# Optimization experiments

Measured on AMD Instinct MI355X. Metric: run time of the kernel, lower is better.

The kernel has to match this reference:

```python
import jax, jax.numpy as jnp
import numpy as np

B, T, I, H, L = 64, 1024, 64, 512, 2


def setup_inputs() -> dict:
    key = jax.random.key(0)
    ks = jax.random.split(key, 4 * L + 4)
    k = 1.0 / np.sqrt(H)
    inp = {"x": jax.random.normal(ks[0], (B, T, I), dtype=jnp.float32)}
    in_sizes = [I] + [H] * (L - 1)
    for l in range(L):
        base = 1 + 4 * l
        inp[f"w_ih{l}"] = jax.random.uniform(ks[base + 0], (3 * H, in_sizes[l]), minval=-k, maxval=k, dtype=jnp.float32)
        inp[f"w_hh{l}"] = jax.random.uniform(ks[base + 1], (3 * H, H), minval=-k, maxval=k, dtype=jnp.float32)
        inp[f"b_ih{l}"] = jax.random.uniform(ks[base + 2], (3 * H,), minval=-k, maxval=k, dtype=jnp.float32)
        inp[f"b_hh{l}"] = jax.random.uniform(ks[base + 3], (3 * H,), minval=-k, maxval=k, dtype=jnp.float32)
    kf = 1.0 / np.sqrt(H)
    inp["fc_w"] = jax.random.uniform(ks[-2], (I, H), minval=-kf, maxval=kf, dtype=jnp.float32)
    inp["fc_b"] = jax.random.uniform(ks[-1], (I,), minval=-kf, maxval=kf, dtype=jnp.float32)
    return inp


def _gru_layer(x, w_ih, w_hh, b_ih, b_hh):
    # x: [B, T, in]; precompute input-side gates as one big GEMM
    xg = jnp.einsum('bti,gi->btg', x, w_ih) + b_ih  # [B, T, 3H]
    h0 = jnp.zeros((x.shape[0], w_hh.shape[1]), x.dtype)

    def step(h, xg_t):
        hg = h @ w_hh.T + b_hh                     # [B, 3H]
        xr, xz, xn = jnp.split(xg_t, 3, axis=-1)
        hr, hz, hn = jnp.split(hg, 3, axis=-1)
        r = jax.nn.sigmoid(xr + hr)
        z = jax.nn.sigmoid(xz + hz)
        n = jnp.tanh(xn + r * hn)
        h_new = (1.0 - z) * n + z * h
        return h_new, h_new

    _, ys = jax.lax.scan(step, h0, jnp.swapaxes(xg, 0, 1))  # ys: [T, B, H]
    return jnp.swapaxes(ys, 0, 1)


def reference(x, w_ih0, w_hh0, b_ih0, b_hh0, w_ih1, w_hh1, b_ih1, b_hh1, fc_w, fc_b):
    h = _gru_layer(x, w_ih0, w_hh0, b_ih0, b_hh0)
    h = _gru_layer(h, w_ih1, w_hh1, b_ih1, b_hh1)
    return h @ fc_w.T + fc_b
```

## Files before the change

### kernel.cpp

```cpp
#include <hip/hip_runtime.h>
#include <hip/hip_bf16.h>

#define T_TOTAL 1024
#define BATCH   64
#define HID     512

__device__ __forceinline__ float fast_sigmoid(float x) {
    return 1.f / (1.f + __expf(-x));
}
__device__ __forceinline__ float fast_tanh(float x) {
    float ax = fabsf(x);
    float e  = __expf(-2.f * ax);
    float t  = (1.f - e) / (1.f + e);
    return copysignf(t, x);
}

template<int BM, int BN, int TM, int TN>
__global__ __launch_bounds__(256, 2)
void gemm_bt_k(const float* __restrict__ A, const float* __restrict__ W,
               const float* __restrict__ bias, float* __restrict__ C,
               int K, int T, int Tc, int t0, int N)
{
    constexpr int BK = 16;
    constexpr int WSTR = BN + (BN / 32) * 4;
    static_assert(BM / TM == 16 && BN / TN == 16, "256 threads required");
    __shared__ float As[BK][BM + 4];
    __shared__ float Ws[BK][WSTR];

    const int tid = threadIdx.x;
    const int tx  = tid & 15;
    const int ty  = tid >> 4;
    const int m0  = blockIdx.y * BM;
    const int n0  = blockIdx.x * BN;
    const int nA  = tx * TN;
    const int nsw = nA + ((nA >> 5) << 2);

    float acc[TM][TN];
#pragma unroll
    for (int i = 0; i < TM; ++i)
#pragma unroll
        for (int j = 0; j < TN; ++j) acc[i][j] = 0.f;

    for (int k0 = 0; k0 < K; k0 += BK) {
#pragma unroll
        for (int i = 0; i < (BM * BK) / 1024; ++i) {
            int id = tid + (i << 8);
            int m  = id >> 2;
            int kq = (id & 3) << 2;
            int mloc = m0 + m;
            int rowg = (mloc / Tc) * T + t0 + (mloc % Tc);
            const float4 v = *reinterpret_cast<const float4*>(A + (size_t)rowg * K + k0 + kq);
            As[kq + 0][m] = v.x; As[kq + 1][m] = v.y;
            As[kq + 2][m] = v.z; As[kq + 3][m] = v.w;
        }
#pragma unroll
        for (int i = 0; i < (BN * BK) / 1024; ++i) {
            int id = tid + (i << 8);
            int n  = id >> 2;
            int kq = (id & 3) << 2;
            const float4 v = *reinterpret_cast<const float4*>(W + (size_t)(n0 + n) * K + k0 + kq);
            int np = n + ((n >> 5) << 2);
            Ws[kq + 0][np] = v.x; Ws[kq + 1][np] = v.y;
            Ws[kq + 2][np] = v.z; Ws[kq + 3][np] = v.w;
        }
        __syncthreads();
#pragma unroll
        for (int k = 0; k < BK; ++k) {
            float a[TM], b[TN];
#pragma unroll
            for (int i = 0; i < TM; i += 4)
                *reinterpret_cast<float4*>(&a[i]) =
                    *reinterpret_cast<const float4*>(&As[k][ty * TM + i]);
#pragma unroll
            for (int j = 0; j < TN; j += 4)
                *reinterpret_cast<float4*>(&b[j]) =
                    *reinterpret_cast<const float4*>(&Ws[k][nsw + j]);
#pragma unroll
            for (int i = 0; i < TM; ++i)
#pragma unroll
                for (int j = 0; j < TN; ++j)
                    acc[i][j] = fmaf(a[i], b[j], acc[i][j]);
        }
        __syncthreads();
    }
#pragma unroll
    for (int i = 0; i < TM; ++i) {
        const size_t crow = (size_t)(m0 + ty * TM + i) * N + n0 + nA;
#pragma unroll
        for (int j = 0; j < TN; j += 4) {
            float4 bv = *reinterpret_cast<const float4*>(bias + n0 + nA + j);
            float4 v;
            v.x = acc[i][j + 0] + bv.x; v.y = acc[i][j + 1] + bv.y;
            v.z = acc[i][j + 2] + bv.z; v.w = acc[i][j + 3] + bv.w;
            *reinterpret_cast<float4*>(C + crow + j) = v;
        }
    }
}

__global__ __launch_bounds__(512, 2)
void gru_scan(const float* __restrict__ xg,
              const float* __restrict__ w_hh,
              const float* __restrict__ b_hh,
              float* __restrict__ y,
              unsigned long long* __restrict__ hbuf,
              int t0, int Tc, int tagbase)
{
    const int tid = threadIdx.x;
    const int grp = blockIdx.x & 31;
    const int os  = blockIdx.x >> 5;
    const int D0  = os << 6;
    const int d   = tid & 63;
    const int kc  = tid >> 6;
    const int bg  = grp << 1;

    constexpr int HP = 528;
    __shared__ float h_lds[2][2 * HP];
    __shared__ float part[8 * 392];
    __shared__ float hg_red[392];

    float4 w4[3][16];
#pragma unroll
    for (int g = 0; g < 3; ++g) {
        const float* wr = w_hh + (size_t)(g * 512 + D0 + d) * 512 + kc * 64;
#pragma unroll
        for (int j = 0; j < 16; ++j)
            w4[g][j] = *reinterpret_cast<const float4*>(wr + (j << 2));
    }
    float bias0 = (tid < 384) ? b_hh[(tid >> 7) * 512 + D0 + (tid & 63)] : 0.f;
    const int b_loc = tid >> 6;

    for (int tl = 0; tl < Tc; ++tl) {
        const int tg = t0 + tl;
        float* hl = h_lds[tl & 1];

        float xr = 0.f, xz = 0.f, xn = 0.f;
        if (tid < 128) {
            const size_t rowo = ((size_t)(bg + b_loc) * Tc + tl) * 1536 + D0 + d;
            xr = xg[rowo];
            xz = xg[rowo + 512];
            xn = xg[rowo + 1024];
        }

        if (tg == 0) {
#pragma unroll
            for (int i = 0; i < 2; ++i) {
                int idx = tid + (i << 9);
                hl[(idx >> 9) * HP + (idx & 511)] = 0.f;
            }
        } else {
            const unsigned long long* hsrc =
                hbuf + (size_t)(grp * 2 + ((tg - 1) & 1)) * 1024;
            const unsigned int tagexp = (unsigned int)(tagbase + tl - 1);
            unsigned long long v[2];
            unsigned int pend = 0x3u;
            while (pend) {
#pragma unroll
                for (int i = 0; i < 2; ++i)
                    if (pend & (1u << i))
                        v[i] = __hip_atomic_load(hsrc + tid + (i << 9),
                                __ATOMIC_RELAXED, __HIP_MEMORY_SCOPE_AGENT);
#pragma unroll
                for (int i = 0; i < 2; ++i)
                    if ((pend & (1u << i)) &&
                        (unsigned int)(v[i] >> 32) == tagexp) {
                        int idx = tid + (i << 9);
                        union { unsigned int u; float f; } cv;
                        cv.u = (unsigned int)v[i];
                        hl[(idx >> 9) * HP + (idx & 511)] = cv.f;
                        pend &= ~(1u << i);
                    }
                if (pend) __builtin_amdgcn_s_sleep(1);
            }
        }
        __syncthreads();

        float acc[3][2];
#pragma unroll
        for (int g = 0; g < 3; ++g) { acc[g][0] = 0.f; acc[g][1] = 0.f; }
        const float* hb_base = hl + kc * 64;
#pragma unroll
        for (int j = 0; j < 16; ++j) {
            const float4 h0 = *reinterpret_cast<const float4*>(hb_base + (j << 2));
            const float4 h1 = *reinterpret_cast<const float4*>(hb_base + HP + (j << 2));
#pragma unroll
            for (int g = 0; g < 3; ++g) {
                const float4 wv = w4[g][j];
                acc[g][0] = fmaf(wv.x, h0.x, acc[g][0]);
                acc[g][0] = fmaf(wv.y, h0.y, acc[g][0]);
                acc[g][0] = fmaf(wv.z, h0.z, acc[g][0]);
                acc[g][0] = fmaf(wv.w, h0.w, acc[g][0]);
                acc[g][1] = fmaf(wv.x, h1.x, acc[g][1]);
                acc[g][1] = fmaf(wv.y, h1.y, acc[g][1]);
                acc[g][1] = fmaf(wv.z, h1.z, acc[g][1]);
                acc[g][1] = fmaf(wv.w, h1.w, acc[g][1]);
            }
        }
        {
            float* pp = part + kc * 392 + d;
#pragma unroll
            for (int g = 0; g < 3; ++g) {
                pp[g * 128]      = acc[g][0];
                pp[g * 128 + 64] = acc[g][1];
            }
        }
        __syncthreads();

        if (tid < 384) {
            float s = bias0;
#pragma unroll
            for (int q = 0; q < 8; ++q) s += part[q * 392 + tid];
            hg_red[tid] = s;
        }
        __syncthreads();

        if (tid < 128) {
            const float hr = hg_red[tid];
            const float hz = hg_red[128 + tid];
            const float hn = hg_red[256 + tid];
            const int D = D0 + d;
            const float hp = hl[b_loc * HP + D];
            const float r = fast_sigmoid(xr + hr);
            const float z = fast_sigmoid(xz + hz);
            const float nv = fast_tanh(xn + r * hn);
            const float h = (1.f - z) * nv + z * hp;
            union { float f; unsigned int u; } cv; cv.f = h;
            const unsigned long long pk =
                ((unsigned long long)(unsigned int)(tagbase + tl) << 32) | cv.u;
            unsigned long long* hdst =
                hbuf + (size_t)(grp * 2 + (tg & 1)) * 1024 + b_loc * 512 + D;
            __hip_atomic_store(hdst, pk, __ATOMIC_RELAXED,
                               __HIP_MEMORY_SCOPE_AGENT);
            y[((size_t)(bg + b_loc) * T_TOTAL + tg) * HID + D] = h;
        }
    }
}

extern "C" void kernel_launch(void* const* d_in, const int* in_sizes, int n_in,
                              void* d_out, int out_size, void* d_ws, size_t ws_size,
                              hipStream_t stream)
{
    const float* x       = (const float*)d_in[0];
    const float* w_ih[2] = {(const float*)d_in[1], (const float*)d_in[5]};
    const float* w_hh[2] = {(const float*)d_in[2], (const float*)d_in[6]};
    const float* b_ih[2] = {(const float*)d_in[3], (const float*)d_in[7]};
    const float* b_hh[2] = {(const float*)d_in[4], (const float*)d_in[8]};
    const float* fc_w    = (const float*)d_in[9];
    const float* fc_b    = (const float*)d_in[10];
    float* out = (float*)d_out;

    const size_t Y_BYTES = (size_t)BATCH * T_TOTAL * HID * 4;
    const size_t H_BYTES = (size_t)32 * 2 * 2 * 512 * 8;
    int Tc = 256;
    while (Tc > 32) {
        size_t need = (size_t)BATCH * Tc * 1536 * 4 + Y_BYTES + H_BYTES;
        if (need <= ws_size) break;
        Tc >>= 1;
    }

    char* p = (char*)d_ws;
    float* xg_buf = (float*)p;                 p += (size_t)BATCH * Tc * 1536 * 4;
    float* y_buf  = (float*)p;                 p += Y_BYTES;
    unsigned long long* hbuf = (unsigned long long*)p;

    const int nchunks = T_TOTAL / Tc;
    for (int L = 0; L < 2; ++L) {
        const float* A = L ? y_buf : x;
        const int K    = L ? HID : 64;
        for (int c = 0; c < nchunks; ++c) {
            dim3 g1(1536 / 128, (BATCH * Tc) / 128);
            gemm_bt_k<128, 128, 8, 8><<<g1, 256, 0, stream>>>(
                A, w_ih[L], b_ih[L], xg_buf, K, T_TOTAL, Tc, c * Tc, 1536);
            gru_scan<<<256, 512, 0, stream>>>(
                xg_buf, w_hh[L], b_hh[L], y_buf, hbuf,
                c * Tc, Tc, (L << 11) + c * Tc);
        }
    }
    dim3 g2(64 / 64, (BATCH * T_TOTAL) / 128);
    gemm_bt_k<128, 64, 8, 4><<<g2, 256, 0, stream>>>(
        y_buf, fc_w, fc_b, out, HID, BATCH * T_TOTAL, BATCH * T_TOTAL, 0, 64);
}
```

Measured before the change: 6.952 ms.

## Add per-group arrival counter for scan sync and fold gate reduction into epilogue

Adds a per-group atomic arrival counter. Each gate-computing wavefront increments it after its stores have drained. One thread per block spins on the counter with s_sleep before the rest of the block reads the tagged hidden state, which is meant to cut heavy polling traffic on hbuf. The separate 384-thread partial-sum reduction and its __syncthreads are also removed: the 128 gate threads now sum all three gates' partials themselves. The trade-off is an extra block barrier and sleep latency on the critical path of every timestep, plus more serial work on the gate threads.

```diff
diff --git a/kernel.cpp b/kernel.cpp
--- a/kernel.cpp
+++ b/kernel.cpp
@@ -103,7 +103,8 @@
               const float* __restrict__ b_hh,
               float* __restrict__ y,
               unsigned long long* __restrict__ hbuf,
-              int t0, int Tc, int tagbase)
+              unsigned int* __restrict__ cnt,
+              int t0, int Tc, int tagbase, unsigned int cntbase)
 {
     const int tid = threadIdx.x;
     const int grp = blockIdx.x & 31;
@@ -116,7 +117,6 @@
     constexpr int HP = 528;
     __shared__ float h_lds[2][2 * HP];
     __shared__ float part[8 * 392];
-    __shared__ float hg_red[392];
 
     float4 w4[3][16];
 #pragma unroll
@@ -126,8 +126,14 @@
         for (int j = 0; j < 16; ++j)
             w4[g][j] = *reinterpret_cast<const float4*>(wr + (j << 2));
     }
-    float bias0 = (tid < 384) ? b_hh[(tid >> 7) * 512 + D0 + (tid & 63)] : 0.f;
+    float bias_r = 0.f, bias_z = 0.f, bias_n = 0.f;
+    if (tid < 128) {
+        bias_r = b_hh[       D0 + (tid & 63)];
+        bias_z = b_hh[ 512 + D0 + (tid & 63)];
+        bias_n = b_hh[1024 + D0 + (tid & 63)];
+    }
     const int b_loc = tid >> 6;
+    unsigned int* cptr = cnt + grp * 32;
 
     for (int tl = 0; tl < Tc; ++tl) {
         const int tg = t0 + tl;
@@ -148,6 +154,15 @@
                 hl[(idx >> 9) * HP + (idx & 511)] = 0.f;
             }
         } else {
+            if (tid == 0) {
+                const unsigned int tgt = cntbase + 16u * (unsigned int)tl;
+                while (__hip_atomic_load(cptr, __ATOMIC_RELAXED,
+                                         __HIP_MEMORY_SCOPE_AGENT) < tgt) {
+                    __builtin_amdgcn_s_sleep(1);
+                }
+            }
+            __syncthreads();
+
             const unsigned long long* hsrc =
                 hbuf + (size_t)(grp * 2 + ((tg - 1) & 1)) * 1024;
             const unsigned int tagexp = (unsigned int)(tagbase + tl - 1);
@@ -205,24 +220,20 @@
         }
         __syncthreads();
 
-        if (tid < 384) {
-            float s = bias0;
-#pragma unroll
-            for (int q = 0; q < 8; ++q) s += part[q * 392 + tid];
-            hg_red[tid] = s;
-        }
-        __syncthreads();
-
         if (tid < 128) {
-            const float hr = hg_red[tid];
-            const float hz = hg_red[128 + tid];
-            const float hn = hg_red[256 + tid];
+            float sr = bias_r, sz = bias_z, sn = bias_n;
+#pragma unroll
+            for (int q = 0; q < 8; ++q) {
+                sr += part[q * 392 +       tid];
+                sz += part[q * 392 + 128 + tid];
+                sn += part[q * 392 + 256 + tid];
+            }
             const int D = D0 + d;
             const float hp = hl[b_loc * HP + D];
-            const float r = fast_sigmoid(xr + hr);
-            const float z = fast_sigmoid(xz + hz);
-            const float nv = fast_tanh(xn + r * hn);
-            const float h = (1.f - z) * nv + z * hp;
+            const float r  = fast_sigmoid(xr + sr);
+            const float z  = fast_sigmoid(xz + sz);
+            const float nv = fast_tanh(xn + r * sn);
+            const float h  = (1.f - z) * nv + z * hp;
             union { float f; unsigned int u; } cv; cv.f = h;
             const unsigned long long pk =
                 ((unsigned long long)(unsigned int)(tagbase + tl) << 32) | cv.u;
@@ -231,6 +242,12 @@
             __hip_atomic_store(hdst, pk, __ATOMIC_RELAXED,
                                __HIP_MEMORY_SCOPE_AGENT);
             y[((size_t)(bg + b_loc) * T_TOTAL + tg) * HID + D] = h;
+            __builtin_amdgcn_sched_barrier(0);
+            __builtin_amdgcn_s_waitcnt(0x0F70);
+            __builtin_amdgcn_sched_barrier(0);
+            if ((tid & 63) == 0)
+                __hip_atomic_fetch_add(cptr, 1u, __ATOMIC_RELAXED,
+                                       __HIP_MEMORY_SCOPE_AGENT);
         }
     }
 }
@@ -250,9 +267,10 @@
 
     const size_t Y_BYTES = (size_t)BATCH * T_TOTAL * HID * 4;
     const size_t H_BYTES = (size_t)32 * 2 * 2 * 512 * 8;
+    const size_t C_BYTES = (size_t)32 * 32 * 4;
     int Tc = 256;
     while (Tc > 32) {
-        size_t need = (size_t)BATCH * Tc * 1536 * 4 + Y_BYTES + H_BYTES;
+        size_t need = (size_t)BATCH * Tc * 1536 * 4 + Y_BYTES + H_BYTES + C_BYTES;
         if (need <= ws_size) break;
         Tc >>= 1;
     }
@@ -260,7 +278,10 @@
     char* p = (char*)d_ws;
     float* xg_buf = (float*)p;                 p += (size_t)BATCH * Tc * 1536 * 4;
     float* y_buf  = (float*)p;                 p += Y_BYTES;
-    unsigned long long* hbuf = (unsigned long long*)p;
+    unsigned long long* hbuf = (unsigned long long*)p; p += H_BYTES;
+    unsigned int* cnt = (unsigned int*)p;
+
+    hipMemsetAsync(cnt, 0, C_BYTES, stream);
 
     const int nchunks = T_TOTAL / Tc;
     for (int L = 0; L < 2; ++L) {
@@ -270,9 +291,11 @@
             dim3 g1(1536 / 128, (BATCH * Tc) / 128);
             gemm_bt_k<128, 128, 8, 8><<<g1, 256, 0, stream>>>(
                 A, w_ih[L], b_ih[L], xg_buf, K, T_TOTAL, Tc, c * Tc, 1536);
+            const int epoch = L * nchunks + c;
             gru_scan<<<256, 512, 0, stream>>>(
-                xg_buf, w_hh[L], b_hh[L], y_buf, hbuf,
-                c * Tc, Tc, (L << 11) + c * Tc);
+                xg_buf, w_hh[L], b_hh[L], y_buf, hbuf, cnt,
+                c * Tc, Tc, (L << 11) + c * Tc,
+                (unsigned int)(epoch * 16 * Tc));
         }
     }
     dim3 g2(64 / 64, (BATCH * T_TOTAL) / 128);
```

After: 7.704 ms. 1.11x slower.

## Drop block barriers in GRU scan with wave-local h loads and double-buffered partials

Applied to the files above, without the earlier changes.

Each wave now polls and stores only the 64-element slice of the previous hidden state that it consumes itself. This lets the barrier after the h load be replaced by a wait on outstanding memory counters. The partial-sum buffer is double-buffered, and the cross-wave reduction is folded into the gate threads, which removes the separate reduction stage and its extra barrier. The goal is fewer block-wide synchronisations per timestep in this latency-bound recurrence. The cost is that 128 threads now each do 24 serial LDS reads, and the LDS padding used to avoid bank conflicts is gone.

```diff
diff --git a/kernel.cpp b/kernel.cpp
--- a/kernel.cpp
+++ b/kernel.cpp
@@ -113,10 +113,8 @@
     const int kc  = tid >> 6;
     const int bg  = grp << 1;
 
-    constexpr int HP = 528;
-    __shared__ float h_lds[2][2 * HP];
-    __shared__ float part[8 * 392];
-    __shared__ float hg_red[392];
+    __shared__ float h_lds[2][1024];
+    __shared__ float part[2][8 * 392];
 
     float4 w4[3][16];
 #pragma unroll
@@ -126,12 +124,18 @@
         for (int j = 0; j < 16; ++j)
             w4[g][j] = *reinterpret_cast<const float4*>(wr + (j << 2));
     }
-    float bias0 = (tid < 384) ? b_hh[(tid >> 7) * 512 + D0 + (tid & 63)] : 0.f;
+    float bias_r = 0.f, bias_z = 0.f, bias_n = 0.f;
+    if (tid < 128) {
+        bias_r = b_hh[       D0 + d];
+        bias_z = b_hh[ 512 + D0 + d];
+        bias_n = b_hh[1024 + D0 + d];
+    }
     const int b_loc = tid >> 6;
 
     for (int tl = 0; tl < Tc; ++tl) {
         const int tg = t0 + tl;
         float* hl = h_lds[tl & 1];
+        float* pt = part[tl & 1];
 
         float xr = 0.f, xz = 0.f, xn = 0.f;
         if (tid < 128) {
@@ -142,46 +146,44 @@
         }
 
         if (tg == 0) {
-#pragma unroll
-            for (int i = 0; i < 2; ++i) {
-                int idx = tid + (i << 9);
-                hl[(idx >> 9) * HP + (idx & 511)] = 0.f;
-            }
+            hl[      kc * 64 + d] = 0.f;
+            hl[512 + kc * 64 + d] = 0.f;
         } else {
             const unsigned long long* hsrc =
-                hbuf + (size_t)(grp * 2 + ((tg - 1) & 1)) * 1024;
+                hbuf + (size_t)(grp * 2 + ((tg - 1) & 1)) * 1024 + kc * 64;
             const unsigned int tagexp = (unsigned int)(tagbase + tl - 1);
-            unsigned long long v[2];
+            unsigned long long v0 = 0, v1 = 0;
             unsigned int pend = 0x3u;
             while (pend) {
-#pragma unroll
-                for (int i = 0; i < 2; ++i)
-                    if (pend & (1u << i))
-                        v[i] = __hip_atomic_load(hsrc + tid + (i << 9),
-                                __ATOMIC_RELAXED, __HIP_MEMORY_SCOPE_AGENT);
-#pragma unroll
-                for (int i = 0; i < 2; ++i)
-                    if ((pend & (1u << i)) &&
-                        (unsigned int)(v[i] >> 32) == tagexp) {
-                        int idx = tid + (i << 9);
-                        union { unsigned int u; float f; } cv;
-                        cv.u = (unsigned int)v[i];
-                        hl[(idx >> 9) * HP + (idx & 511)] = cv.f;
-                        pend &= ~(1u << i);
-                    }
+                if (pend & 1u)
+                    v0 = __hip_atomic_load(hsrc + d,
+                            __ATOMIC_RELAXED, __HIP_MEMORY_SCOPE_AGENT);
+                if (pend & 2u)
+                    v1 = __hip_atomic_load(hsrc + 512 + d,
+                            __ATOMIC_RELAXED, __HIP_MEMORY_SCOPE_AGENT);
+                if ((pend & 1u) && (unsigned int)(v0 >> 32) == tagexp) {
+                    union { unsigned int u; float f; } cv; cv.u = (unsigned int)v0;
+                    hl[kc * 64 + d] = cv.f;
+                    pend &= ~1u;
+                }
+                if ((pend & 2u) && (unsigned int)(v1 >> 32) == tagexp) {
+                    union { unsigned int u; float f; } cv; cv.u = (unsigned int)v1;
+                    hl[512 + kc * 64 + d] = cv.f;
+                    pend &= ~2u;
+                }
                 if (pend) __builtin_amdgcn_s_sleep(1);
             }
         }
-        __syncthreads();
+        __builtin_amdgcn_s_waitcnt(0xC07F);
 
         float acc[3][2];
 #pragma unroll
         for (int g = 0; g < 3; ++g) { acc[g][0] = 0.f; acc[g][1] = 0.f; }
-        const float* hb_base = hl + kc * 64;
+        const float* hb = hl + kc * 64;
 #pragma unroll
         for (int j = 0; j < 16; ++j) {
-            const float4 h0 = *reinterpret_cast<const float4*>(hb_base + (j << 2));
-            const float4 h1 = *reinterpret_cast<const float4*>(hb_base + HP + (j << 2));
+            const float4 h0 = *reinterpret_cast<const float4*>(hb + (j << 2));
+            const float4 h1 = *reinterpret_cast<const float4*>(hb + 512 + (j << 2));
 #pragma unroll
             for (int g = 0; g < 3; ++g) {
                 const float4 wv = w4[g][j];
@@ -196,7 +198,7 @@
             }
         }
         {
-            float* pp = part + kc * 392 + d;
+            float* pp = pt + kc * 392 + d;
 #pragma unroll
             for (int g = 0; g < 3; ++g) {
                 pp[g * 128]      = acc[g][0];
@@ -205,24 +207,20 @@
         }
         __syncthreads();
 
-        if (tid < 384) {
-            float s = bias0;
-#pragma unroll
-            for (int q = 0; q < 8; ++q) s += part[q * 392 + tid];
-            hg_red[tid] = s;
-        }
-        __syncthreads();
-
         if (tid < 128) {
-            const float hr = hg_red[tid];
-            const float hz = hg_red[128 + tid];
-            const float hn = hg_red[256 + tid];
+            float sr = bias_r, sz = bias_z, sn = bias_n;
+#pragma unroll
+            for (int q = 0; q < 8; ++q) {
+                sr += pt[q * 392 +       tid];
+                sz += pt[q * 392 + 128 + tid];
+                sn += pt[q * 392 + 256 + tid];
+            }
             const int D = D0 + d;
-            const float hp = hl[b_loc * HP + D];
-            const float r = fast_sigmoid(xr + hr);
-            const float z = fast_sigmoid(xz + hz);
-            const float nv = fast_tanh(xn + r * hn);
-            const float h = (1.f - z) * nv + z * hp;
+            const float hp = hl[b_loc * 512 + D];
+            const float r  = fast_sigmoid(xr + sr);
+            const float z  = fast_sigmoid(xz + sz);
+            const float nv = fast_tanh(xn + r * sn);
+            const float h  = (1.f - z) * nv + z * hp;
             union { float f; unsigned int u; } cv; cv.f = h;
             const unsigned long long pk =
                 ((unsigned long long)(unsigned int)(tagbase + tl) << 32) | cv.u;
```

Result: faster. 6.391 ms (-8.1%).
